# Kernel optimization log

Measured on AMD Instinct MI355X. Metric: run time of the kernel, lower is better.

The kernel has to match this reference:

```python
import jax, jax.numpy as jnp
import numpy as np

DEPTH = 9            # perfect binary tree depth (root=level 0, leaves=level DEPTH)
N_TREES = 128
H = 256              # h_size == x_size (ndata['h'] init uses x_size)
NPT = 2 ** (DEPTH + 1) - 1   # 1023 nodes per tree
N = N_TREES * NPT            # 130944 total nodes


def _levels():
    """Static per-level (node, left-child, right-child) global index arrays."""
    base = np.arange(N_TREES, dtype=np.int64)[:, None] * NPT
    out = []
    for l in range(DEPTH + 1):
        loc = np.arange(2 ** l - 1, 2 ** (l + 1) - 1, dtype=np.int64)
        nodes = (base + loc[None, :]).reshape(-1)
        if l < DEPTH:
            cl = (base + (2 * loc + 1)[None, :]).reshape(-1)
            cr = (base + (2 * loc + 2)[None, :]).reshape(-1)
        else:
            cl = cr = None
        out.append((jnp.asarray(nodes),
                    None if cl is None else jnp.asarray(cl),
                    None if cr is None else jnp.asarray(cr)))
    return out


def setup_inputs() -> dict:
    key = jax.random.key(0)
    ks = jax.random.split(key, 10)
    s = lambda d: 1.0 / np.sqrt(d)
    return {
        "wordid": jax.random.randint(ks[0], (N,), 0, 32000),
        "mask":   jax.random.randint(ks[1], (N,), 0, 2),
        "emb":    jax.random.normal(ks[2], (32000, H), jnp.float32) * 0.02,
        "W_iou":  jax.random.normal(ks[3], (H, 3 * H), jnp.float32) * s(H),
        "U_iou":  jax.random.normal(ks[4], (2 * H, 3 * H), jnp.float32) * s(2 * H),
        "U_f_w":  jax.random.normal(ks[5], (2 * H, 2 * H), jnp.float32) * s(2 * H),
        "U_f_b":  jax.random.normal(ks[6], (2 * H,), jnp.float32) * 0.01,
        "b_iou":  jax.random.normal(ks[7], (3 * H,), jnp.float32) * 0.01,
        "lin_w":  jax.random.normal(ks[8], (H, 4), jnp.float32) * s(H),
        "lin_b":  jax.random.normal(ks[9], (4,), jnp.float32) * 0.01,
    }


def _apply_node(iou, b_iou, c_in, mh_in):
    i, o, u = jnp.split(iou + b_iou, 3, axis=1)
    i, o, u = jax.nn.sigmoid(i), jax.nn.sigmoid(o), jnp.tanh(u)
    c = i * u + c_in
    h = o * jnp.tanh(c)
    return h, c, jnp.maximum(h, mh_in)


def reference(wordid, mask, emb, W_iou, U_iou, U_f_w, U_f_b, b_iou, lin_w, lin_b):
    levels = _levels()
    x = emb[wordid * mask]                                  # [N, H]
    iou0 = (x @ W_iou) * mask[:, None].astype(x.dtype)      # leaf/pre-set iou [N, 3H]

    h = jnp.zeros((N, H), x.dtype)
    c = jnp.zeros((N, H), x.dtype)
    mh = jnp.zeros((N, H), x.dtype)

    # leaves: no incoming messages -> apply with preset iou, c=0, max_h=0
    li, _, _ = levels[DEPTH]
    hh, cc, mm = _apply_node(iou0[li], b_iou, 0.0, 0.0)
    h, c, mh = h.at[li].set(hh), c.at[li].set(cc), mh.at[li].set(mm)

    # internal levels, bottom-up (DGL prop_nodes_topo)
    for l in range(DEPTH - 1, -1, -1):
        ni, cl, cr = levels[l]
        h_cat = jnp.concatenate([h[cl], h[cr]], axis=1)     # [M, 2H]
        f = jax.nn.sigmoid(h_cat @ U_f_w + U_f_b)           # [M, 2H]
        fl, fr = jnp.split(f, 2, axis=1)
        c_red = fl * c[cl] + fr * c[cr]
        mh_red = jnp.maximum(mh[cl], mh[cr])
        iou = h_cat @ U_iou                                  # overwrites preset iou
        hh, cc, mm = _apply_node(iou, b_iou, c_red, mh_red)
        h, c, mh = h.at[ni].set(hh), c.at[ni].set(cc), mh.at[ni].set(mm)

    return (h + mh) @ lin_w + lin_b                         # logits [N, num_classes]
```

## Files before the change

kernel.cpp:

```cpp
#include <hip/hip_runtime.h>
#include <hip/hip_bf16.h>


#define NTREES 128
#define NPT    1023
#define HS     256
#define NNODES (NTREES * NPT)
#define NL     (NTREES * 512)

typedef __hip_bfloat16 bf16;
typedef unsigned short us8 __attribute__((ext_vector_type(8)));
typedef unsigned short us4 __attribute__((ext_vector_type(4)));
typedef short bf16x8 __attribute__((ext_vector_type(8)));
typedef float f32x4 __attribute__((ext_vector_type(4)));

typedef __attribute__((address_space(1))) const void gvoid;
typedef __attribute__((address_space(3))) void svoid;
#define GLD16(gp, lp) \
    __builtin_amdgcn_global_load_lds((gvoid*)(gp), (svoid*)(lp), 16, 0, 0)

__device__ __forceinline__ float bits2f(unsigned short b) {
    return __uint_as_float(((unsigned)b) << 16);
}
__device__ __forceinline__ unsigned short f2bits(float x) {
    bf16 h = __float2bfloat16(x);
    return *reinterpret_cast<unsigned short*>(&h);
}
__device__ __forceinline__ float fsigm(float x) {
    return __builtin_amdgcn_rcpf(1.0f + __expf(-x));
}
__device__ __forceinline__ float ftanh(float x) {
    return 1.0f - 2.0f * __builtin_amdgcn_rcpf(1.0f + __expf(2.0f * x));
}

#define WT_ELEMS (768 * 256)
#define UT_ELEMS (1280 * 512)

__global__ __launch_bounds__(256) void prep_w(
    const float* __restrict__ W_iou, const float* __restrict__ U_f_w,
    const float* __restrict__ U_iou, bf16* __restrict__ Wt, bf16* __restrict__ Ut)
{
    const int i = blockIdx.x * 256 + threadIdx.x;
    if (i < WT_ELEMS) {
        const int n = i >> 8, k = i & 255;
        Wt[i] = __float2bfloat16(W_iou[k * 768 + n]);
    } else if (i < WT_ELEMS + UT_ELEMS) {
        const int j = i - WT_ELEMS;
        const int n = j >> 9, k = j & 511;
        const float v = (n < 512) ? U_f_w[k * 512 + n] : U_iou[k * 768 + (n - 512)];
        Ut[j] = __float2bfloat16(v);
    }
}

__global__ __launch_bounds__(256) void gather_x(
    const int* __restrict__ wordid, const int* __restrict__ mask,
    const float* __restrict__ emb, bf16* __restrict__ x_bf)
{
    const int wave = threadIdx.x >> 6, lane = threadIdx.x & 63;
    const int gr   = blockIdx.x * 4 + wave;
    const int node = (gr >> 9) * NPT + 511 + (gr & 511);
    const int j0   = lane * 4;
    us4 v;
    if (mask[node]) {
        const float4 f = *(const float4*)(emb + (long)wordid[node] * HS + j0);
        v[0] = f2bits(f.x); v[1] = f2bits(f.y);
        v[2] = f2bits(f.z); v[3] = f2bits(f.w);
    } else {
        v[0] = v[1] = v[2] = v[3] = 0;
    }
    *(us4*)(x_bf + (long)gr * HS + j0) = v;
}

__global__ __launch_bounds__(256) void leaf_fused(
    const bf16* __restrict__ x_bf, const bf16* __restrict__ Wt,
    const float* __restrict__ b_iou,
    bf16* __restrict__ h_s, bf16* __restrict__ cm_s,
    bf16* __restrict__ s_full, const int tree0)
{
    __shared__ __align__(16) short a_s[2][128 * 32];
    __shared__ __align__(16) short b_s[2][128 * 32];
    const int t    = threadIdx.x;
    const int bm0  = blockIdx.x * 128;
    const int c0   = blockIdx.y * 32;
    const int lane = t & 63, wave = t >> 6;
    const int l4a = lane >> 2, k8 = (lane & 3) * 8;

    const bf16* aSrc[2];
    #pragma unroll
    for (int q = 0; q < 2; ++q) {
        const int row = (wave * 2 + q) * 16 + l4a;
        aSrc[q] = x_bf + (long)(tree0 * 512 + bm0 + row) * HS + k8;
    }
    const bf16* bSrc[2];
    #pragma unroll
    for (int q = 0; q < 2; ++q) {
        int rb = (wave * 2 + q) * 16 + l4a;
        if (rb > 95) rb = 95;
        const int g = rb >> 5, jl = rb & 31;
        bSrc[q] = Wt + (long)(g * 256 + c0 + jl) * 256 + k8;
    }

    const int wr = wave >> 1, wc = wave & 1;
    const int fr = lane & 15, l4 = lane >> 4;

    f32x4 acc[4][3];
    #pragma unroll
    for (int i = 0; i < 4; ++i)
        #pragma unroll
        for (int g = 0; g < 3; ++g) acc[i][g] = (f32x4){0.f, 0.f, 0.f, 0.f};

    auto stage = [&](int buf, int step) {
        const int kt = step * 32;
        #pragma unroll
        for (int q = 0; q < 2; ++q)
            GLD16(aSrc[q] + kt, &a_s[buf][(wave * 2 + q) * 512]);
        #pragma unroll
        for (int q = 0; q < 2; ++q)
            GLD16(bSrc[q] + kt, &b_s[buf][(wave * 2 + q) * 512]);
    };

    stage(0, 0);
    stage(1, 1);
    int cur = 0;
    for (int it = 0; it < 8; ++it) {
        if (it < 7) { asm volatile("s_waitcnt vmcnt(4)" ::: "memory"); }
        else        { asm volatile("s_waitcnt vmcnt(0)" ::: "memory"); }
        __builtin_amdgcn_sched_barrier(0);
        __builtin_amdgcn_s_barrier();
        __builtin_amdgcn_sched_barrier(0);
        bf16x8 af[4], bg[3];
        #pragma unroll
        for (int i = 0; i < 4; ++i)
            af[i] = *(const bf16x8*)&a_s[cur][(wr * 64 + i * 16 + fr) * 32 + l4 * 8];
        #pragma unroll
        for (int g = 0; g < 3; ++g)
            bg[g] = *(const bf16x8*)&b_s[cur][(g * 32 + wc * 16 + fr) * 32 + l4 * 8];
        #pragma unroll
        for (int i = 0; i < 4; ++i)
            #pragma unroll
            for (int g = 0; g < 3; ++g)
                acc[i][g] = __builtin_amdgcn_mfma_f32_16x16x32_bf16(
                    bg[g], af[i], acc[i][g], 0, 0, 0);
        __builtin_amdgcn_s_barrier();
        __builtin_amdgcn_sched_barrier(0);
        if (it < 6) stage(cur, it + 2);
        cur ^= 1;
    }

    const int j0 = c0 + wc * 16 + l4 * 4;
    const float4 bi4 = *(const float4*)(b_iou + j0);
    const float4 bo4 = *(const float4*)(b_iou + 256 + j0);
    const float4 bu4 = *(const float4*)(b_iou + 512 + j0);
    #pragma unroll
    for (int i = 0; i < 4; ++i) {
        const int r    = bm0 + wr * 64 + i * 16 + fr;
        const int gr   = tree0 * 512 + r;
        const int node = (gr >> 9) * NPT + 511 + (gr & 511);
        us4 sh, ss; us8 scm;
        #pragma unroll
        for (int q = 0; q < 4; ++q) {
            const float iv = fsigm(acc[i][0][q] + ((const float*)&bi4)[q]);
            const float ov = fsigm(acc[i][1][q] + ((const float*)&bo4)[q]);
            const float uv = ftanh(acc[i][2][q] + ((const float*)&bu4)[q]);
            const float cv  = iv * uv;
            const float hv  = ov * ftanh(cv);
            const float mhv = fmaxf(hv, 0.0f);
            sh[q] = f2bits(hv); ss[q] = f2bits(hv + mhv);
            scm[2 * q] = f2bits(cv); scm[2 * q + 1] = f2bits(mhv);
        }
        *(us4*)(h_s + (long)r * HS + j0)        = sh;
        *(us8*)(cm_s + (long)r * 512 + j0 * 2)  = scm;
        *(us4*)(s_full + (long)node * HS + j0)  = ss;
    }
}

__global__ __launch_bounds__(256) void level_fused(
    const bf16* __restrict__ h_child, const bf16* __restrict__ cm_c,
    const bf16* __restrict__ Ut,
    const float* __restrict__ U_f_b, const float* __restrict__ b_iou,
    bf16* __restrict__ h_p, bf16* __restrict__ cm_p,
    bf16* __restrict__ s_full, const int lvl, const int M, const int tree0)
{
    __shared__ __align__(16) short a_s[2][128 * 32];
    __shared__ __align__(16) short b_s[2][192 * 32];
    const int t    = threadIdx.x;
    const int bm0  = blockIdx.x * 128;
    const int c0   = blockIdx.y * 32;
    const int lane = t & 63, wave = t >> 6;
    const int l4a = lane >> 2, k8 = (lane & 3) * 8;

    const bf16* aSrc[2];
    #pragma unroll
    for (int q = 0; q < 2; ++q) {
        int p = bm0 + (wave * 2 + q) * 16 + l4a;
        if (p >= M) p = M - 1;
        const int tl  = p >> lvl;
        const int idx = p & ((1 << lvl) - 1);
        const int cls = tl * (2 << lvl) + 2 * idx;
        aSrc[q] = h_child + (long)cls * HS + k8;
    }
    const bf16* bSrc[3];
    #pragma unroll
    for (int q = 0; q < 3; ++q) {
        int rb = (wave * 3 + q) * 16 + l4a;
        if (rb > 159) rb = 159;
        const int g = rb >> 5, jl = rb & 31;
        bSrc[q] = Ut + (long)(g * 256 + c0 + jl) * 512 + k8;
    }

    const int wr = wave >> 1, wc = wave & 1;
    const int fr = lane & 15, l4 = lane >> 4;

    f32x4 acc[4][5];
    #pragma unroll
    for (int i = 0; i < 4; ++i)
        #pragma unroll
        for (int g = 0; g < 5; ++g) acc[i][g] = (f32x4){0.f, 0.f, 0.f, 0.f};

    auto stage = [&](int buf, int step) {
        const int kt = step * 32;
        #pragma unroll
        for (int q = 0; q < 2; ++q)
            GLD16(aSrc[q] + kt, &a_s[buf][(wave * 2 + q) * 512]);
        #pragma unroll
        for (int q = 0; q < 3; ++q)
            GLD16(bSrc[q] + kt, &b_s[buf][(wave * 3 + q) * 512]);
    };

    stage(0, 0);
    stage(1, 1);
    int cur = 0;
    for (int it = 0; it < 16; ++it) {
        if (it < 15) { asm volatile("s_waitcnt vmcnt(5)" ::: "memory"); }
        else         { asm volatile("s_waitcnt vmcnt(0)" ::: "memory"); }
        __builtin_amdgcn_sched_barrier(0);
        __builtin_amdgcn_s_barrier();
        __builtin_amdgcn_sched_barrier(0);
        bf16x8 af[4], bg[5];
        #pragma unroll
        for (int i = 0; i < 4; ++i)
            af[i] = *(const bf16x8*)&a_s[cur][(wr * 64 + i * 16 + fr) * 32 + l4 * 8];
        #pragma unroll
        for (int g = 0; g < 5; ++g)
            bg[g] = *(const bf16x8*)&b_s[cur][(g * 32 + wc * 16 + fr) * 32 + l4 * 8];
        #pragma unroll
        for (int i = 0; i < 4; ++i)
            #pragma unroll
            for (int g = 0; g < 5; ++g)
                acc[i][g] = __builtin_amdgcn_mfma_f32_16x16x32_bf16(
                    bg[g], af[i], acc[i][g], 0, 0, 0);
        __builtin_amdgcn_s_barrier();
        __builtin_amdgcn_sched_barrier(0);
        if (it < 14) stage(cur, it + 2);
        cur ^= 1;
    }

    const int j0 = c0 + wc * 16 + l4 * 4;
    const float4 bfl4 = *(const float4*)(U_f_b + j0);
    const float4 bfr4 = *(const float4*)(U_f_b + 256 + j0);
    const float4 bi4  = *(const float4*)(b_iou + j0);
    const float4 bo4  = *(const float4*)(b_iou + 256 + j0);
    const float4 bu4  = *(const float4*)(b_iou + 512 + j0);
    #pragma unroll
    for (int i = 0; i < 4; ++i) {
        const int r  = bm0 + wr * 64 + i * 16 + fr;
        const int rc = r < M ? r : M - 1;
        const int tl   = rc >> lvl;
        const int idx  = rc & ((1 << lvl) - 1);
        const int cls  = tl * (2 << lvl) + 2 * idx;
        const int node = (tree0 + tl) * NPT + (1 << lvl) - 1 + idx;
        const us8 cml = *(const us8*)(cm_c + (long)cls * 512 + j0 * 2);
        const us8 cmr = *(const us8*)(cm_c + (long)(cls + 1) * 512 + j0 * 2);
        us4 sh, ss; us8 scm;
        #pragma unroll
        for (int q = 0; q < 4; ++q) {
            const float flv = fsigm(acc[i][0][q] + ((const float*)&bfl4)[q]);
            const float frv = fsigm(acc[i][1][q] + ((const float*)&bfr4)[q]);
            const float iv  = fsigm(acc[i][2][q] + ((const float*)&bi4)[q]);
            const float ov  = fsigm(acc[i][3][q] + ((const float*)&bo4)[q]);
            const float uv  = ftanh(acc[i][4][q] + ((const float*)&bu4)[q]);
            const float ccl = bits2f(cml[2 * q]), mhl = bits2f(cml[2 * q + 1]);
            const float ccr = bits2f(cmr[2 * q]), mhr = bits2f(cmr[2 * q + 1]);
            const float cv  = iv * uv + flv * ccl + frv * ccr;
            const float hv  = ov * ftanh(cv);
            const float mhv = fmaxf(hv, fmaxf(mhl, mhr));
            sh[q] = f2bits(hv); ss[q] = f2bits(hv + mhv);
            scm[2 * q] = f2bits(cv); scm[2 * q + 1] = f2bits(mhv);
        }
        if (r < M) {
            *(us4*)(h_p + (long)r * HS + j0)       = sh;
            *(us8*)(cm_p + (long)r * 512 + j0 * 2) = scm;
            *(us4*)(s_full + (long)node * HS + j0) = ss;
        }
    }
}

__global__ __launch_bounds__(256) void logits_k(
    const bf16* __restrict__ s_full, const float* __restrict__ lin_w,
    const float* __restrict__ lin_b, float* __restrict__ out)
{
    const int wave = threadIdx.x >> 6, lane = threadIdx.x & 63;
    const int node = blockIdx.x * 4 + wave;
    const int j0   = lane * 4;
    const us4 v = *(const us4*)(s_full + (long)node * HS + j0);
    float p0 = 0.f, p1 = 0.f, p2 = 0.f, p3 = 0.f;
    #pragma unroll
    for (int q = 0; q < 4; ++q) {
        const float s  = bits2f(v[q]);
        const float4 w = *(const float4*)(lin_w + (j0 + q) * 4);
        p0 += s * w.x; p1 += s * w.y; p2 += s * w.z; p3 += s * w.w;
    }
    #pragma unroll
    for (int m = 1; m < 64; m <<= 1) {
        p0 += __shfl_xor(p0, m); p1 += __shfl_xor(p1, m);
        p2 += __shfl_xor(p2, m); p3 += __shfl_xor(p3, m);
    }
    if (lane == 0) {
        float4 r;
        r.x = p0 + lin_b[0]; r.y = p1 + lin_b[1];
        r.z = p2 + lin_b[2]; r.w = p3 + lin_b[3];
        *(float4*)(out + (long)node * 4) = r;
    }
}

extern "C" void kernel_launch(void* const* d_in, const int* in_sizes, int n_in,
                              void* d_out, int out_size, void* d_ws, size_t ws_size,
                              hipStream_t stream) {
    const int*   wordid = (const int*)d_in[0];
    const int*   mask   = (const int*)d_in[1];
    const float* emb    = (const float*)d_in[2];
    const float* W_iou  = (const float*)d_in[3];
    const float* U_iou  = (const float*)d_in[4];
    const float* U_f_w  = (const float*)d_in[5];
    const float* U_f_b  = (const float*)d_in[6];
    const float* b_iou  = (const float*)d_in[7];
    const float* lin_w  = (const float*)d_in[8];
    const float* lin_b  = (const float*)d_in[9];
    float* out = (float*)d_out;

    const size_t wElems = (size_t)WT_ELEMS + UT_ELEMS;
    const size_t sElems = (size_t)NNODES * HS;
    const size_t xElems = (size_t)NL * HS;
    auto need = [&](int T) -> size_t {
        return (wElems + sElems + xElems + (size_t)T * 589824) * 2;
    };
    int T = 8;
    const int cands[4] = {128, 64, 32, 16};
    for (int ci = 0; ci < 4; ++ci) {
        if (need(cands[ci]) <= ws_size) { T = cands[ci]; break; }
    }

    bf16* Wt     = (bf16*)d_ws;
    bf16* Ut     = Wt + WT_ELEMS;
    bf16* s_full = Ut + UT_ELEMS;
    bf16* x_bf   = s_full + sElems;
    bf16* hA  = x_bf + xElems;
    bf16* cmA = hA  + (size_t)T * 512 * HS;
    bf16* hB  = cmA + (size_t)T * 512 * HS * 2;
    bf16* cmB = hB  + (size_t)T * 256 * HS;

    prep_w<<<(int)((wElems + 255) / 256), 256, 0, stream>>>(
        W_iou, U_f_w, U_iou, Wt, Ut);
    gather_x<<<NL / 4, 256, 0, stream>>>(wordid, mask, emb, x_bf);

    for (int tree0 = 0; tree0 < NTREES; tree0 += T) {
        leaf_fused<<<dim3(T * 512 / 128, 8), 256, 0, stream>>>(
            x_bf, Wt, b_iou, hA, cmA, s_full, tree0);
        bool childIsA = true;
        for (int l = 8; l >= 0; --l) {
            bf16 *hc, *cmc, *hp, *cmp;
            if (childIsA) { hc = hA; cmc = cmA; hp = hB; cmp = cmB; }
            else          { hc = hB; cmc = cmB; hp = hA; cmp = cmA; }
            const int M = T << l;
            level_fused<<<dim3((M + 127) / 128, 8), 256, 0, stream>>>(
                hc, cmc, Ut, U_f_b, b_iou, hp, cmp, s_full, l, M, tree0);
            childIsA = !childIsA;
        }
    }
    logits_k<<<NNODES / 4, 256, 0, stream>>>(s_full, lin_w, lin_b, out);
}
```

Measured before the change: 426.7 us.

## Merge prep kernels, trim redundant B-tile loads, simplify GEMM double-buffering

```diff
diff --git a/kernel.cpp b/kernel.cpp
--- a/kernel.cpp
+++ b/kernel.cpp
@@ -35,29 +35,32 @@
 
 #define WT_ELEMS (768 * 256)
 #define UT_ELEMS (1280 * 512)
-
-__global__ __launch_bounds__(256) void prep_w(
+#define PW_ELEMS (WT_ELEMS + UT_ELEMS)
+#define PREPB    ((PW_ELEMS + 255) / 256)
+
+__global__ __launch_bounds__(256) void prep_all(
     const float* __restrict__ W_iou, const float* __restrict__ U_f_w,
-    const float* __restrict__ U_iou, bf16* __restrict__ Wt, bf16* __restrict__ Ut)
+    const float* __restrict__ U_iou,
+    const int* __restrict__ wordid, const int* __restrict__ mask,
+    const float* __restrict__ emb,
+    bf16* __restrict__ Wt, bf16* __restrict__ Ut, bf16* __restrict__ x_bf)
 {
-    const int i = blockIdx.x * 256 + threadIdx.x;
-    if (i < WT_ELEMS) {
-        const int n = i >> 8, k = i & 255;
-        Wt[i] = __float2bfloat16(W_iou[k * 768 + n]);
-    } else if (i < WT_ELEMS + UT_ELEMS) {
-        const int j = i - WT_ELEMS;
-        const int n = j >> 9, k = j & 511;
-        const float v = (n < 512) ? U_f_w[k * 512 + n] : U_iou[k * 768 + (n - 512)];
-        Ut[j] = __float2bfloat16(v);
-    }
-}
-
-__global__ __launch_bounds__(256) void gather_x(
-    const int* __restrict__ wordid, const int* __restrict__ mask,
-    const float* __restrict__ emb, bf16* __restrict__ x_bf)
-{
+    if (blockIdx.x < PREPB) {
+        const int i = blockIdx.x * 256 + threadIdx.x;
+        if (i < WT_ELEMS) {
+            const int n = i >> 8, k = i & 255;
+            Wt[i] = __float2bfloat16(W_iou[k * 768 + n]);
+        } else if (i < PW_ELEMS) {
+            const int j = i - WT_ELEMS;
+            const int n = j >> 9, k = j & 511;
+            const float v = (n < 512) ? U_f_w[k * 512 + n]
+                                      : U_iou[k * 768 + (n - 512)];
+            Ut[j] = __float2bfloat16(v);
+        }
+        return;
+    }
     const int wave = threadIdx.x >> 6, lane = threadIdx.x & 63;
-    const int gr   = blockIdx.x * 4 + wave;
+    const int gr   = (blockIdx.x - PREPB) * 4 + wave;
     const int node = (gr >> 9) * NPT + 511 + (gr & 511);
     const int j0   = lane * 4;
     us4 v;
@@ -78,7 +81,7 @@
     bf16* __restrict__ s_full, const int tree0)
 {
     __shared__ __align__(16) short a_s[2][128 * 32];
-    __shared__ __align__(16) short b_s[2][128 * 32];
+    __shared__ __align__(16) short b_s[2][96 * 32];
     const int t    = threadIdx.x;
     const int bm0  = blockIdx.x * 128;
     const int c0   = blockIdx.y * 32;
@@ -91,10 +94,12 @@
         const int row = (wave * 2 + q) * 16 + l4a;
         aSrc[q] = x_bf + (long)(tree0 * 512 + bm0 + row) * HS + k8;
     }
+    const int bCnt = (wave < 3) ? 2 : 0;
+    const int bStart = wave * 2;
     const bf16* bSrc[2];
     #pragma unroll
     for (int q = 0; q < 2; ++q) {
-        int rb = (wave * 2 + q) * 16 + l4a;
+        int rb = (bStart + q) * 16 + l4a;
         if (rb > 95) rb = 95;
         const int g = rb >> 5, jl = rb & 31;
         bSrc[q] = Wt + (long)(g * 256 + c0 + jl) * 256 + k8;
@@ -109,25 +114,21 @@
         #pragma unroll
         for (int g = 0; g < 3; ++g) acc[i][g] = (f32x4){0.f, 0.f, 0.f, 0.f};
 
-    auto stage = [&](int buf, int step) {
-        const int kt = step * 32;
+    auto stage = [&](int buf, int kt) {
         #pragma unroll
         for (int q = 0; q < 2; ++q)
             GLD16(aSrc[q] + kt, &a_s[buf][(wave * 2 + q) * 512]);
         #pragma unroll
         for (int q = 0; q < 2; ++q)
-            GLD16(bSrc[q] + kt, &b_s[buf][(wave * 2 + q) * 512]);
+            if (q < bCnt) GLD16(bSrc[q] + kt, &b_s[buf][(bStart + q) * 512]);
     };
 
     stage(0, 0);
-    stage(1, 1);
+    __syncthreads();
     int cur = 0;
-    for (int it = 0; it < 8; ++it) {
-        if (it < 7) { asm volatile("s_waitcnt vmcnt(4)" ::: "memory"); }
-        else        { asm volatile("s_waitcnt vmcnt(0)" ::: "memory"); }
-        __builtin_amdgcn_sched_barrier(0);
-        __builtin_amdgcn_s_barrier();
-        __builtin_amdgcn_sched_barrier(0);
+    for (int kt = 0; kt < 256; kt += 32) {
+        const int nk = kt + 32;
+        if (nk < 256) stage(cur ^ 1, nk);
         bf16x8 af[4], bg[3];
         #pragma unroll
         for (int i = 0; i < 4; ++i)
@@ -141,9 +142,7 @@
             for (int g = 0; g < 3; ++g)
                 acc[i][g] = __builtin_amdgcn_mfma_f32_16x16x32_bf16(
                     bg[g], af[i], acc[i][g], 0, 0, 0);
-        __builtin_amdgcn_s_barrier();
-        __builtin_amdgcn_sched_barrier(0);
-        if (it < 6) stage(cur, it + 2);
+        __syncthreads();
         cur ^= 1;
     }
 
@@ -182,7 +181,7 @@
     bf16* __restrict__ s_full, const int lvl, const int M, const int tree0)
 {
     __shared__ __align__(16) short a_s[2][128 * 32];
-    __shared__ __align__(16) short b_s[2][192 * 32];
+    __shared__ __align__(16) short b_s[2][160 * 32];
     const int t    = threadIdx.x;
     const int bm0  = blockIdx.x * 128;
     const int c0   = blockIdx.y * 32;
@@ -199,10 +198,12 @@
         const int cls = tl * (2 << lvl) + 2 * idx;
         aSrc[q] = h_child + (long)cls * HS + k8;
     }
+    const int bCnt   = (wave < 2) ? 3 : 2;
+    const int bStart = (wave < 2) ? wave * 3 : 6 + (wave - 2) * 2;
     const bf16* bSrc[3];
     #pragma unroll
     for (int q = 0; q < 3; ++q) {
-        int rb = (wave * 3 + q) * 16 + l4a;
+        int rb = (bStart + q) * 16 + l4a;
         if (rb > 159) rb = 159;
         const int g = rb >> 5, jl = rb & 31;
         bSrc[q] = Ut + (long)(g * 256 + c0 + jl) * 512 + k8;
@@ -217,25 +218,21 @@
         #pragma unroll
         for (int g = 0; g < 5; ++g) acc[i][g] = (f32x4){0.f, 0.f, 0.f, 0.f};
 
-    auto stage = [&](int buf, int step) {
-        const int kt = step * 32;
+    auto stage = [&](int buf, int kt) {
         #pragma unroll
         for (int q = 0; q < 2; ++q)
             GLD16(aSrc[q] + kt, &a_s[buf][(wave * 2 + q) * 512]);
         #pragma unroll
         for (int q = 0; q < 3; ++q)
-            GLD16(bSrc[q] + kt, &b_s[buf][(wave * 3 + q) * 512]);
+            if (q < bCnt) GLD16(bSrc[q] + kt, &b_s[buf][(bStart + q) * 512]);
     };
 
     stage(0, 0);
-    stage(1, 1);
+    __syncthreads();
     int cur = 0;
-    for (int it = 0; it < 16; ++it) {
-        if (it < 15) { asm volatile("s_waitcnt vmcnt(5)" ::: "memory"); }
-        else         { asm volatile("s_waitcnt vmcnt(0)" ::: "memory"); }
-        __builtin_amdgcn_sched_barrier(0);
-        __builtin_amdgcn_s_barrier();
-        __builtin_amdgcn_sched_barrier(0);
+    for (int kt = 0; kt < 512; kt += 32) {
+        const int nk = kt + 32;
+        if (nk < 512) stage(cur ^ 1, nk);
         bf16x8 af[4], bg[5];
         #pragma unroll
         for (int i = 0; i < 4; ++i)
@@ -249,9 +246,7 @@
             for (int g = 0; g < 5; ++g)
                 acc[i][g] = __builtin_amdgcn_mfma_f32_16x16x32_bf16(
                     bg[g], af[i], acc[i][g], 0, 0, 0);
-        __builtin_amdgcn_s_barrier();
-        __builtin_amdgcn_sched_barrier(0);
-        if (it < 14) stage(cur, it + 2);
+        __syncthreads();
         cur ^= 1;
     }
 
@@ -338,7 +333,7 @@
     const float* lin_b  = (const float*)d_in[9];
     float* out = (float*)d_out;
 
-    const size_t wElems = (size_t)WT_ELEMS + UT_ELEMS;
+    const size_t wElems = (size_t)PW_ELEMS;
     const size_t sElems = (size_t)NNODES * HS;
     const size_t xElems = (size_t)NL * HS;
     auto need = [&](int T) -> size_t {
@@ -359,9 +354,8 @@
     bf16* hB  = cmA + (size_t)T * 512 * HS * 2;
     bf16* cmB = hB  + (size_t)T * 256 * HS;
 
-    prep_w<<<(int)((wElems + 255) / 256), 256, 0, stream>>>(
-        W_iou, U_f_w, U_iou, Wt, Ut);
-    gather_x<<<NL / 4, 256, 0, stream>>>(wordid, mask, emb, x_bf);
+    prep_all<<<PREPB + NL / 4, 256, 0, stream>>>(
+        W_iou, U_f_w, U_iou, wordid, mask, emb, Wt, Ut, x_bf);
 
     for (int tree0 = 0; tree0 < NTREES; tree0 += T) {
         leaf_fused<<<dim3(T * 512 / 128, 8), 256, 0, stream>>>(
```

Result: no change. 422.8 us (-0.9%).
